# Kernel optimization log

Hardware: AMD Instinct MI355X
Metric: run time of the kernel (lower is better)

## Reference

```python
import jax, jax.numpy as jnp
import numpy as np

EPS = 1e-12  # torch F.normalize eps
K = 32       # num_clusters (hardcoded in module)

def l2norm(v, axis):
    n = jnp.sqrt(jnp.sum(v * v, axis=axis, keepdims=True))
    return v / jnp.maximum(n, EPS)

def setup_inputs() -> dict:
    key = jax.random.key(0)
    k1, k2, k3, k4 = jax.random.split(key, 4)
    B, M, D = 64, 128, 2048
    x = jax.random.normal(k1, (B, M, D), dtype=jnp.float32)
    # ragged lengths in [1, M]
    lengths = jax.random.randint(k2, (B,), 0, M, dtype=jnp.int32) + 1
    init_sc = 1.0 / np.sqrt(D)
    W = init_sc * jax.random.normal(k3, (K, D), dtype=jnp.float32)  # fc1.weight
    C = init_sc * jax.random.normal(k4, (K, D), dtype=jnp.float32)  # centroids
    return {"x": x, "lengths": lengths, "W": W, "C": C}

def reference(x, lengths, W, C):
    # x: [B,M,D] padded frames, lengths: [B] valid frame counts
    B, M, D = x.shape
    mask = (jnp.arange(M)[None, :] < lengths[:, None]).astype(x.dtype)  # [B,M]
    cnt = lengths.astype(x.dtype)[:, None]                              # [B,1]
    # avg pooling over valid (raw, un-normalized) frames
    avgpool = jnp.sum(x * mask[:, :, None], axis=1) / cnt               # [B,D]
    # per-frame L2 normalize
    xn = l2norm(x, axis=-1)                                             # [B,M,D]
    # soft assignment: linear (no bias) + softmax over clusters
    logits = jnp.einsum('bmd,kd->bmk', xn, W)
    a = jax.nn.softmax(logits, axis=-1) * mask[:, :, None]              # [B,M,K]
    # VLAD residual aggregation, GEMM form:
    # sum_m a[b,m,k]*(xn[b,m,:] - C[k,:]) = (a^T xn) - C * sum_m a
    ax = jnp.einsum('bmk,bmd->bkd', a, xn)                              # [B,K,D]
    asum = jnp.sum(a, axis=1)                                           # [B,K]
    vlad = ax - asum[:, :, None] * C[None, :, :]                        # [B,K,D]
    # intra-normalize per cluster, flatten, global L2 normalize
    vlad = l2norm(vlad, axis=2)
    vlad = vlad.reshape(B, K * D)
    vlad = l2norm(vlad, axis=1)
    return jnp.concatenate([avgpool, vlad], axis=1)                     # [B, D + K*D]
```

## Files before the change

### kernel.cpp

```cpp
#include <hip/hip_runtime.h>
#include <math.h>

#define BB 64
#define MM 128
#define DDIM 2048
#define KK 32
#define NDC 16
#define OUTROW (DDIM + KK*DDIM)

typedef __attribute__((ext_vector_type(8))) short bf16x8;
typedef __attribute__((ext_vector_type(4))) float f32x4;

__device__ __forceinline__ short f2bf(float f) {
  unsigned u = __builtin_bit_cast(unsigned, f);
  u += 0x7fffu + ((u >> 16) & 1u);
  return (short)(u >> 16);
}
__device__ __forceinline__ unsigned pack2(float lo, float hi) {
  return (unsigned)(unsigned short)f2bf(lo) | ((unsigned)(unsigned short)f2bf(hi) << 16);
}

__global__ __launch_bounds__(256) void k_prep(const float* __restrict__ W,
                                              short* __restrict__ Wb) {
  int i = (blockIdx.x * 256 + threadIdx.x) * 8;
  float4 a = *(const float4*)(W + i);
  float4 b = *(const float4*)(W + i + 4);
  bf16x8 o = {f2bf(a.x), f2bf(a.y), f2bf(a.z), f2bf(a.w),
              f2bf(b.x), f2bf(b.y), f2bf(b.z), f2bf(b.w)};
  *(bf16x8*)(Wb + i) = o;
}

__global__ __launch_bounds__(512, 4) void k_logits(const float* __restrict__ x,
    const int* __restrict__ lengths, const short* __restrict__ Wb,
    short* __restrict__ aT, float* __restrict__ asum_p) {
  const int t = threadIdx.x, wv = t >> 6, lane = t & 63;
  const int l15 = lane & 15, quad = lane >> 4;
  const int fg = blockIdx.x;
  const int g0 = fg * 16;
  const int b  = fg >> 3;
  const int m0 = (fg & 7) * 16;
  const int len = lengths[b];

  if (m0 >= len) {
    if (t < KK) asum_p[(size_t)fg * KK + t] = 0.f;
    if (t < 256) {
      const int zk = t >> 3, zoff = (t & 7) * 2;
      *(unsigned*)(aT + (size_t)b * KK * MM + (size_t)zk * MM + m0 + zoff) = 0u;
    }
    return;
  }

  const bool av = (m0 + l15) < len;
  const float* xrow = x + (size_t)(g0 + l15) * DDIM + wv * 256 + quad * 8;
  const short* w0   = Wb + l15 * DDIM + wv * 256 + quad * 8;
  const short* w1   = w0 + 16 * DDIM;

  f32x4 c0 = {0.f, 0.f, 0.f, 0.f}, c1 = {0.f, 0.f, 0.f, 0.f};
  float ssq = 0.f;
  {
    float4 xa[8], xc[8];
    bf16x8 B0[8], B1[8];
    #pragma unroll
    for (int s = 0; s < 8; ++s) {
      if (av) {
        xa[s] = *(const float4*)(xrow + s * 32);
        xc[s] = *(const float4*)(xrow + s * 32 + 4);
      } else {
        xa[s] = make_float4(0.f, 0.f, 0.f, 0.f);
        xc[s] = make_float4(0.f, 0.f, 0.f, 0.f);
      }
      B0[s] = *(const bf16x8*)(w0 + s * 32);
      B1[s] = *(const bf16x8*)(w1 + s * 32);
    }
    #pragma unroll
    for (int s = 0; s < 8; ++s) {
      ssq = fmaf(xa[s].x, xa[s].x, ssq); ssq = fmaf(xa[s].y, xa[s].y, ssq);
      ssq = fmaf(xa[s].z, xa[s].z, ssq); ssq = fmaf(xa[s].w, xa[s].w, ssq);
      ssq = fmaf(xc[s].x, xc[s].x, ssq); ssq = fmaf(xc[s].y, xc[s].y, ssq);
      ssq = fmaf(xc[s].z, xc[s].z, ssq); ssq = fmaf(xc[s].w, xc[s].w, ssq);
      bf16x8 A = {f2bf(xa[s].x), f2bf(xa[s].y), f2bf(xa[s].z), f2bf(xa[s].w),
                  f2bf(xc[s].x), f2bf(xc[s].y), f2bf(xc[s].z), f2bf(xc[s].w)};
      c0 = __builtin_amdgcn_mfma_f32_16x16x32_bf16(A, B0[s], c0, 0, 0, 0);
      c1 = __builtin_amdgcn_mfma_f32_16x16x32_bf16(A, B1[s], c1, 0, 0, 0);
    }
  }

  ssq += __shfl_xor(ssq, 16, 64);
  ssq += __shfl_xor(ssq, 32, 64);
  __shared__ float sq[8][16];
  __shared__ float lg[8][16][33];
  if (quad == 0) sq[wv][l15] = ssq;
  #pragma unroll
  for (int r = 0; r < 4; ++r) {
    lg[wv][quad * 4 + r][l15]      = c0[r];
    lg[wv][quad * 4 + r][16 + l15] = c1[r];
  }
  __syncthreads();

  const int fr = t >> 5, kk = t & 31;
  float s0 = 0.f;
  #pragma unroll
  for (int w = 0; w < 8; ++w) s0 += lg[w][fr][kk];
  float ss = 0.f;
  #pragma unroll
  for (int w = 0; w < 8; ++w) ss += sq[w][fr];
  float inv = 1.f / fmaxf(sqrtf(ss), 1e-12f);
  s0 *= inv;
  float mx = s0;
  mx = fmaxf(mx, __shfl_xor(mx, 1, 32));
  mx = fmaxf(mx, __shfl_xor(mx, 2, 32));
  mx = fmaxf(mx, __shfl_xor(mx, 4, 32));
  mx = fmaxf(mx, __shfl_xor(mx, 8, 32));
  mx = fmaxf(mx, __shfl_xor(mx, 16, 32));
  float e0 = __expf(s0 - mx);
  float se = e0;
  se += __shfl_xor(se, 1, 32);
  se += __shfl_xor(se, 2, 32);
  se += __shfl_xor(se, 4, 32);
  se += __shfl_xor(se, 8, 32);
  se += __shfl_xor(se, 16, 32);
  const bool valid = (m0 + fr) < len;
  float rr = valid ? (1.f / se) : 0.f;
  float a0 = e0 * rr;

  __syncthreads();
  lg[0][fr][kk] = a0;
  __syncthreads();
  if (t < KK) {
    float s = 0.f;
    #pragma unroll
    for (int f = 0; f < 16; ++f) s += lg[0][f][t];
    asum_p[(size_t)fg * KK + t] = s;
  }
  short* ap = aT + (size_t)b * KK * MM + m0 + fr;
  ap[(size_t)kk * MM] = f2bf(a0 * inv);
}

__global__ __launch_bounds__(256, 4) void k_vlad(const float* __restrict__ x,
    const int* __restrict__ lengths, const float* __restrict__ Cc,
    const short* __restrict__ aT, const float* __restrict__ asum_p,
    float* __restrict__ out, float* __restrict__ ssq_part) {
  const int t = threadIdx.x, wv = t >> 6, lane = t & 63;
  const int l15 = lane & 15, quad = lane >> 4;
  const int dc = blockIdx.x, b = blockIdx.y;
  const int dh = wv & 1, mh = wv >> 1;
  const int dwb = dc * 128 + dh * 64;
  const int mb  = mh * 64;
  const int len = lengths[b];

  __shared__ __attribute__((aligned(16))) char ubuf[20480];
  short (*xbt)[64][40]     = (short(*)[64][40])ubuf;
  float (*exch)[2][64][20] = (float(*)[2][64][20])ubuf;
  __shared__ float  asl[KK];
  __shared__ float4 avp[2][16];
  __shared__ float  ssw[4][17];

  if (t < KK) {
    float s = 0.f;
    #pragma unroll
    for (int p = 0; p < 8; ++p) s += asum_p[(size_t)(b * 8 + p) * KK + t];
    asl[t] = s;
  }

  const float* xb  = x  + (size_t)b * MM * DDIM;
  const short* at0 = aT + (size_t)b * KK * MM + l15 * MM + mb + quad * 8;

  const int q4   = l15 * 4;
  const int mrow = quad * 2;
  const int keyw = l15 & 3;
  const int keyr = (l15 >> 2) & 3;

  bf16x8 A0[2], A1[2];
  #pragma unroll
  for (int ms = 0; ms < 2; ++ms) {
    A0[ms] = *(const bf16x8*)(at0 + ms * 32);
    A1[ms] = *(const bf16x8*)(at0 + 16 * MM + ms * 32);
  }

  float4 v0[8], v1[8];
  #pragma unroll
  for (int ms = 0; ms < 2; ++ms) {
    #pragma unroll
    for (int p = 0; p < 4; ++p) {
      const int m = mb + ms * 32 + p * 8 + mrow;
      const float* xr = xb + (size_t)m * DDIM + dwb + q4;
      v0[ms * 4 + p] = (m < len) ? *(const float4*)xr
                                 : make_float4(0.f, 0.f, 0.f, 0.f);
      v1[ms * 4 + p] = (m + 1 < len) ? *(const float4*)(xr + DDIM)
                                     : make_float4(0.f, 0.f, 0.f, 0.f);
    }
  }

  float avg[4] = {0.f, 0.f, 0.f, 0.f};
  #pragma unroll
  for (int i = 0; i < 8; ++i) {
    avg[0] += v0[i].x + v1[i].x;
    avg[1] += v0[i].y + v1[i].y;
    avg[2] += v0[i].z + v1[i].z;
    avg[3] += v0[i].w + v1[i].w;
  }
  #pragma unroll
  for (int c = 0; c < 4; ++c) {
    avg[c] += __shfl_xor(avg[c], 16, 64);
    avg[c] += __shfl_xor(avg[c], 32, 64);
  }
  if (mh == 1 && quad == 0)
    avp[dh][l15] = make_float4(avg[0], avg[1], avg[2], avg[3]);

  f32x4 acc0[4], acc1[4];
  #pragma unroll
  for (int nt = 0; nt < 4; ++nt) {
    acc0[nt] = (f32x4){0.f, 0.f, 0.f, 0.f};
    acc1[nt] = (f32x4){0.f, 0.f, 0.f, 0.f};
  }

  #pragma unroll
  for (int ms = 0; ms < 2; ++ms) {
    #pragma unroll
    for (int p = 0; p < 4; ++p) {
      const int i = ms * 4 + p;
      const int mls = (p ^ keyw) * 8 + mrow;
      *(unsigned*)&xbt[wv][q4 + 0][mls] = pack2(v0[i].x, v1[i].x);
      *(unsigned*)&xbt[wv][q4 + 1][mls] = pack2(v0[i].y, v1[i].y);
      *(unsigned*)&xbt[wv][q4 + 2][mls] = pack2(v0[i].z, v1[i].z);
      *(unsigned*)&xbt[wv][q4 + 3][mls] = pack2(v0[i].w, v1[i].w);
    }
    #pragma unroll
    for (int nt = 0; nt < 4; ++nt) {
      bf16x8 B = *(const bf16x8*)&xbt[wv][nt * 16 + l15][(quad ^ keyr) * 8];
      acc0[nt] = __builtin_amdgcn_mfma_f32_16x16x32_bf16(A0[ms], B, acc0[nt], 0, 0, 0);
      acc1[nt] = __builtin_amdgcn_mfma_f32_16x16x32_bf16(A1[ms], B, acc1[nt], 0, 0, 0);
    }
  }

  f32x4 keep[4], give[4];
  if (mh == 0) {
    #pragma unroll
    for (int nt = 0; nt < 4; ++nt) { keep[nt] = acc0[nt]; give[nt] = acc1[nt]; }
  } else {
    #pragma unroll
    for (int nt = 0; nt < 4; ++nt) { keep[nt] = acc1[nt]; give[nt] = acc0[nt]; }
  }

  __syncthreads();
  #pragma unroll
  for (int nt = 0; nt < 4; ++nt)
    *(f32x4*)&exch[dh][mh][lane][nt * 4] = give[nt];

  if (mh == 0 && quad == 0) {
    float4 pa = avp[dh][l15];
    float rl = 1.f / (float)len;
    *(float4*)(out + (size_t)b * OUTROW + dwb + q4) =
        make_float4((avg[0] + pa.x) * rl, (avg[1] + pa.y) * rl,
                    (avg[2] + pa.z) * rl, (avg[3] + pa.w) * rl);
  }

  __syncthreads();
  #pragma unroll
  for (int nt = 0; nt < 4; ++nt)
    keep[nt] += *(const f32x4*)&exch[dh][1 - mh][lane][nt * 4];

  float* orow = out + (size_t)b * OUTROW + DDIM;
  #pragma unroll
  for (int r = 0; r < 4; ++r) {
    const int k = mh * 16 + quad * 4 + r;
    const float as = asl[k];
    float sqv = 0.f;
    #pragma unroll
    for (int nt = 0; nt < 4; ++nt) {
      const int d = dwb + nt * 16 + l15;
      float v = keep[nt][r] - as * Cc[(size_t)k * DDIM + d];
      orow[(size_t)k * DDIM + d] = v;
      sqv = fmaf(v, v, sqv);
    }
    sqv += __shfl_xor(sqv, 1, 64);
    sqv += __shfl_xor(sqv, 2, 64);
    sqv += __shfl_xor(sqv, 4, 64);
    sqv += __shfl_xor(sqv, 8, 64);
    if (l15 == 0) ssw[wv][quad * 4 + r] = sqv;
  }
  __syncthreads();
  if (t < KK) {
    const int mt = t >> 4, kl = t & 15;
    ssq_part[((size_t)dc * BB + b) * KK + t] = ssw[mt * 2][kl] + ssw[mt * 2 + 1][kl];
  }
}

__global__ __launch_bounds__(256) void k_norm(const float* __restrict__ ssq_part,
    float* __restrict__ out) {
  const int t = threadIdx.x;
  const int k = blockIdx.x;
  const int b = blockIdx.y;
  __shared__ float ssk[32];
  if (t < 32) {
    float sk = 0.f;
    #pragma unroll
    for (int dc = 0; dc < NDC; ++dc)
      sk += ssq_part[((size_t)dc * BB + b) * KK + t];
    ssk[t] = sk;
  }
  __syncthreads();
  float gss = 0.f, iv_own = 0.f;
  #pragma unroll
  for (int kk = 0; kk < 32; ++kk) {
    float nk = sqrtf(ssk[kk]);
    float iv = 1.f / fmaxf(nk, 1e-12f);
    float nn = nk * iv;
    gss += nn * nn;
    if (kk == k) iv_own = iv;
  }
  float sc = iv_own / fmaxf(sqrtf(gss), 1e-12f);
  float* row = out + (size_t)b * OUTROW + DDIM + (size_t)k * DDIM;
  #pragma unroll
  for (int h = 0; h < 2; ++h) {
    float4* p = (float4*)(row + h * 1024 + t * 4);
    float4 v = *p;
    v.x *= sc; v.y *= sc; v.z *= sc; v.w *= sc;
    *p = v;
  }
}

extern "C" void kernel_launch(void* const* d_in, const int* in_sizes, int n_in,
                              void* d_out, int out_size, void* d_ws, size_t ws_size,
                              hipStream_t stream) {
  const float* x       = (const float*)d_in[0];
  const int*   lengths = (const int*)d_in[1];
  const float* W       = (const float*)d_in[2];
  const float* C       = (const float*)d_in[3];
  float* out = (float*)d_out;

  short* Wb     = (short*)d_ws;
  short* aT     = Wb + (size_t)KK * DDIM;
  float* asum_p = (float*)(aT + (size_t)BB * KK * MM);
  float* ssqp   = asum_p + (size_t)512 * KK;

  k_prep  <<<dim3(32),      256, 0, stream>>>(W, Wb);
  k_logits<<<dim3(512),     512, 0, stream>>>(x, lengths, Wb, aT, asum_p);
  k_vlad  <<<dim3(NDC, BB), 256, 0, stream>>>(x, lengths, C, aT, asum_p, out, ssqp);
  k_norm  <<<dim3(KK, BB),  256, 0, stream>>>(ssqp, out);
}
```

Before: 143.1 us.

## Fuse all four kernels into one per-batch kernel

Replaces the prep, logits, vlad and norm kernels with one kernel that runs a single 512-thread block per batch. The block computes the soft assignments into LDS, does the VLAD GEMM with its own assignments, and applies the intra and global normalization in place. This removes three launches and the workspace round trips for the assignments, partial sums and sums of squares. In exchange the grid shrinks to only 64 blocks on a GPU with many more CUs, so each block walks all of D serially and parallelism drops sharply.

```diff
diff --git a/kernel.cpp b/kernel.cpp
--- a/kernel.cpp
+++ b/kernel.cpp
@@ -5,7 +5,6 @@
 #define MM 128
 #define DDIM 2048
 #define KK 32
-#define NDC 16
 #define OUTROW (DDIM + KK*DDIM)
 
 typedef __attribute__((ext_vector_type(8))) short bf16x8;
@@ -20,58 +19,63 @@
   return (unsigned)(unsigned short)f2bf(lo) | ((unsigned)(unsigned short)f2bf(hi) << 16);
 }
 
-__global__ __launch_bounds__(256) void k_prep(const float* __restrict__ W,
-                                              short* __restrict__ Wb) {
-  int i = (blockIdx.x * 256 + threadIdx.x) * 8;
-  float4 a = *(const float4*)(W + i);
-  float4 b = *(const float4*)(W + i + 4);
-  bf16x8 o = {f2bf(a.x), f2bf(a.y), f2bf(a.z), f2bf(a.w),
-              f2bf(b.x), f2bf(b.y), f2bf(b.z), f2bf(b.w)};
-  *(bf16x8*)(Wb + i) = o;
-}
-
-__global__ __launch_bounds__(512, 4) void k_logits(const float* __restrict__ x,
-    const int* __restrict__ lengths, const short* __restrict__ Wb,
-    short* __restrict__ aT, float* __restrict__ asum_p) {
+__global__ __launch_bounds__(512, 2) void k_all(
+    const float* __restrict__ x, const int* __restrict__ lengths,
+    const float* __restrict__ W, const float* __restrict__ Cc,
+    float* __restrict__ out) {
   const int t = threadIdx.x, wv = t >> 6, lane = t & 63;
   const int l15 = lane & 15, quad = lane >> 4;
-  const int fg = blockIdx.x;
-  const int g0 = fg * 16;
-  const int b  = fg >> 3;
-  const int m0 = (fg & 7) * 16;
+  const int b = blockIdx.x;
   const int len = lengths[b];
 
-  if (m0 >= len) {
-    if (t < KK) asum_p[(size_t)fg * KK + t] = 0.f;
-    if (t < 256) {
-      const int zk = t >> 3, zoff = (t & 7) * 2;
-      *(unsigned*)(aT + (size_t)b * KK * MM + (size_t)zk * MM + m0 + zoff) = 0u;
-    }
-    return;
-  }
-
-  const bool av = (m0 + l15) < len;
-  const float* xrow = x + (size_t)(g0 + l15) * DDIM + wv * 256 + quad * 8;
-  const short* w0   = Wb + l15 * DDIM + wv * 256 + quad * 8;
-  const short* w1   = w0 + 16 * DDIM;
-
-  f32x4 c0 = {0.f, 0.f, 0.f, 0.f}, c1 = {0.f, 0.f, 0.f, 0.f};
-  float ssq = 0.f;
+  __shared__ __attribute__((aligned(16))) char ubuf[40960];
+  float (*lg)[16][33] = (float(*)[16][33])ubuf;
+  short (*xbt)[64][40] = (short(*)[64][40])ubuf;
+  __shared__ short a_lds[KK][136];
+  __shared__ float sq[8][16];
+  __shared__ float asum_lds[KK];
+  __shared__ float ssw[8][33];
+  __shared__ float ssk[KK], scl[KK];
+
+  const float* xb = x + (size_t)b * MM * DDIM;
+  const int dwb = wv * 256;
+
+  bf16x8 WB0[8], WB1[8];
   {
-    float4 xa[8], xc[8];
-    bf16x8 B0[8], B1[8];
+    const float* w0 = W + (size_t)l15 * DDIM + dwb + quad * 8;
+    const float* w1 = w0 + (size_t)16 * DDIM;
     #pragma unroll
     for (int s = 0; s < 8; ++s) {
-      if (av) {
-        xa[s] = *(const float4*)(xrow + s * 32);
-        xc[s] = *(const float4*)(xrow + s * 32 + 4);
-      } else {
-        xa[s] = make_float4(0.f, 0.f, 0.f, 0.f);
-        xc[s] = make_float4(0.f, 0.f, 0.f, 0.f);
-      }
-      B0[s] = *(const bf16x8*)(w0 + s * 32);
-      B1[s] = *(const bf16x8*)(w1 + s * 32);
-    }
+      float4 p0 = *(const float4*)(w0 + s * 32);
+      float4 p1 = *(const float4*)(w0 + s * 32 + 4);
+      float4 q0 = *(const float4*)(w1 + s * 32);
+      float4 q1 = *(const float4*)(w1 + s * 32 + 4);
+      WB0[s] = (bf16x8){f2bf(p0.x), f2bf(p0.y), f2bf(p0.z), f2bf(p0.w),
+                        f2bf(p1.x), f2bf(p1.y), f2bf(p1.z), f2bf(p1.w)};
+      WB1[s] = (bf16x8){f2bf(q0.x), f2bf(q0.y), f2bf(q0.z), f2bf(q0.w),
+                        f2bf(q1.x), f2bf(q1.y), f2bf(q1.z), f2bf(q1.w)};
+    }
+  }
+  if (t < KK) asum_lds[t] = 0.f;
+  if (lane < 32) ssw[wv][lane] = 0.f;
+  __syncthreads();
+
+  float4 xa[8], xc[8];
+  {
+    const bool av = l15 < len;
+    const float* xr = xb + (size_t)l15 * DDIM + dwb + quad * 8;
+    #pragma unroll
+    for (int s = 0; s < 8; ++s) {
+      if (av) { xa[s] = *(const float4*)(xr + s * 32);
+                xc[s] = *(const float4*)(xr + s * 32 + 4); }
+      else    { xa[s] = make_float4(0.f, 0.f, 0.f, 0.f);
+                xc[s] = make_float4(0.f, 0.f, 0.f, 0.f); }
+    }
+  }
+  #pragma unroll
+  for (int it = 0; it < 8; ++it) {
+    f32x4 c0 = {0.f, 0.f, 0.f, 0.f}, c1 = {0.f, 0.f, 0.f, 0.f};
+    float ssq = 0.f;
     #pragma unroll
     for (int s = 0; s < 8; ++s) {
       ssq = fmaf(xa[s].x, xa[s].x, ssq); ssq = fmaf(xa[s].y, xa[s].y, ssq);
@@ -80,240 +84,184 @@
       ssq = fmaf(xc[s].z, xc[s].z, ssq); ssq = fmaf(xc[s].w, xc[s].w, ssq);
       bf16x8 A = {f2bf(xa[s].x), f2bf(xa[s].y), f2bf(xa[s].z), f2bf(xa[s].w),
                   f2bf(xc[s].x), f2bf(xc[s].y), f2bf(xc[s].z), f2bf(xc[s].w)};
-      c0 = __builtin_amdgcn_mfma_f32_16x16x32_bf16(A, B0[s], c0, 0, 0, 0);
-      c1 = __builtin_amdgcn_mfma_f32_16x16x32_bf16(A, B1[s], c1, 0, 0, 0);
-    }
-  }
-
-  ssq += __shfl_xor(ssq, 16, 64);
-  ssq += __shfl_xor(ssq, 32, 64);
-  __shared__ float sq[8][16];
-  __shared__ float lg[8][16][33];
-  if (quad == 0) sq[wv][l15] = ssq;
-  #pragma unroll
-  for (int r = 0; r < 4; ++r) {
-    lg[wv][quad * 4 + r][l15]      = c0[r];
-    lg[wv][quad * 4 + r][16 + l15] = c1[r];
-  }
-  __syncthreads();
-
-  const int fr = t >> 5, kk = t & 31;
-  float s0 = 0.f;
-  #pragma unroll
-  for (int w = 0; w < 8; ++w) s0 += lg[w][fr][kk];
-  float ss = 0.f;
-  #pragma unroll
-  for (int w = 0; w < 8; ++w) ss += sq[w][fr];
-  float inv = 1.f / fmaxf(sqrtf(ss), 1e-12f);
-  s0 *= inv;
-  float mx = s0;
-  mx = fmaxf(mx, __shfl_xor(mx, 1, 32));
-  mx = fmaxf(mx, __shfl_xor(mx, 2, 32));
-  mx = fmaxf(mx, __shfl_xor(mx, 4, 32));
-  mx = fmaxf(mx, __shfl_xor(mx, 8, 32));
-  mx = fmaxf(mx, __shfl_xor(mx, 16, 32));
-  float e0 = __expf(s0 - mx);
-  float se = e0;
-  se += __shfl_xor(se, 1, 32);
-  se += __shfl_xor(se, 2, 32);
-  se += __shfl_xor(se, 4, 32);
-  se += __shfl_xor(se, 8, 32);
-  se += __shfl_xor(se, 16, 32);
-  const bool valid = (m0 + fr) < len;
-  float rr = valid ? (1.f / se) : 0.f;
-  float a0 = e0 * rr;
-
-  __syncthreads();
-  lg[0][fr][kk] = a0;
-  __syncthreads();
-  if (t < KK) {
-    float s = 0.f;
-    #pragma unroll
-    for (int f = 0; f < 16; ++f) s += lg[0][f][t];
-    asum_p[(size_t)fg * KK + t] = s;
-  }
-  short* ap = aT + (size_t)b * KK * MM + m0 + fr;
-  ap[(size_t)kk * MM] = f2bf(a0 * inv);
-}
-
-__global__ __launch_bounds__(256, 4) void k_vlad(const float* __restrict__ x,
-    const int* __restrict__ lengths, const float* __restrict__ Cc,
-    const short* __restrict__ aT, const float* __restrict__ asum_p,
-    float* __restrict__ out, float* __restrict__ ssq_part) {
-  const int t = threadIdx.x, wv = t >> 6, lane = t & 63;
-  const int l15 = lane & 15, quad = lane >> 4;
-  const int dc = blockIdx.x, b = blockIdx.y;
-  const int dh = wv & 1, mh = wv >> 1;
-  const int dwb = dc * 128 + dh * 64;
-  const int mb  = mh * 64;
-  const int len = lengths[b];
-
-  __shared__ __attribute__((aligned(16))) char ubuf[20480];
-  short (*xbt)[64][40]     = (short(*)[64][40])ubuf;
-  float (*exch)[2][64][20] = (float(*)[2][64][20])ubuf;
-  __shared__ float  asl[KK];
-  __shared__ float4 avp[2][16];
-  __shared__ float  ssw[4][17];
-
-  if (t < KK) {
-    float s = 0.f;
-    #pragma unroll
-    for (int p = 0; p < 8; ++p) s += asum_p[(size_t)(b * 8 + p) * KK + t];
-    asl[t] = s;
-  }
-
-  const float* xb  = x  + (size_t)b * MM * DDIM;
-  const short* at0 = aT + (size_t)b * KK * MM + l15 * MM + mb + quad * 8;
+      c0 = __builtin_amdgcn_mfma_f32_16x16x32_bf16(A, WB0[s], c0, 0, 0, 0);
+      c1 = __builtin_amdgcn_mfma_f32_16x16x32_bf16(A, WB1[s], c1, 0, 0, 0);
+    }
+    float4 ya[8], yc[8];
+    if (it < 7) {
+      const int mr = (it + 1) * 16 + l15;
+      const bool av = mr < len;
+      const float* xr = xb + (size_t)mr * DDIM + dwb + quad * 8;
+      #pragma unroll
+      for (int s = 0; s < 8; ++s) {
+        if (av) { ya[s] = *(const float4*)(xr + s * 32);
+                  yc[s] = *(const float4*)(xr + s * 32 + 4); }
+        else    { ya[s] = make_float4(0.f, 0.f, 0.f, 0.f);
+                  yc[s] = make_float4(0.f, 0.f, 0.f, 0.f); }
+      }
+    }
+    ssq += __shfl_xor(ssq, 16, 64);
+    ssq += __shfl_xor(ssq, 32, 64);
+    if (quad == 0) sq[wv][l15] = ssq;
+    #pragma unroll
+    for (int r = 0; r < 4; ++r) {
+      lg[wv][quad * 4 + r][l15]      = c0[r];
+      lg[wv][quad * 4 + r][16 + l15] = c1[r];
+    }
+    __syncthreads();
+    {
+      const int fr = t >> 5, kk = t & 31;
+      float s0 = 0.f, ss = 0.f;
+      #pragma unroll
+      for (int w = 0; w < 8; ++w) { s0 += lg[w][fr][kk]; ss += sq[w][fr]; }
+      float inv = 1.f / fmaxf(sqrtf(ss), 1e-12f);
+      s0 *= inv;
+      float mx = s0;
+      mx = fmaxf(mx, __shfl_xor(mx, 1, 32));
+      mx = fmaxf(mx, __shfl_xor(mx, 2, 32));
+      mx = fmaxf(mx, __shfl_xor(mx, 4, 32));
+      mx = fmaxf(mx, __shfl_xor(mx, 8, 32));
+      mx = fmaxf(mx, __shfl_xor(mx, 16, 32));
+      float e0 = __expf(s0 - mx);
+      float se = e0;
+      se += __shfl_xor(se, 1, 32);
+      se += __shfl_xor(se, 2, 32);
+      se += __shfl_xor(se, 4, 32);
+      se += __shfl_xor(se, 8, 32);
+      se += __shfl_xor(se, 16, 32);
+      const bool valid = (it * 16 + fr) < len;
+      float rr = valid ? (1.f / se) : 0.f;
+      float a0 = e0 * rr;
+      atomicAdd(&asum_lds[kk], a0);
+      a_lds[kk][it * 16 + fr] = f2bf(a0 * inv);
+    }
+    __syncthreads();
+    #pragma unroll
+    for (int s = 0; s < 8; ++s) { xa[s] = ya[s]; xc[s] = yc[s]; }
+  }
 
   const int q4   = l15 * 4;
   const int mrow = quad * 2;
   const int keyw = l15 & 3;
   const int keyr = (l15 >> 2) & 3;
-
-  bf16x8 A0[2], A1[2];
+  const float rlen = 1.f / (float)len;
+  float* orow = out + (size_t)b * OUTROW + DDIM;
+
   #pragma unroll
-  for (int ms = 0; ms < 2; ++ms) {
-    A0[ms] = *(const bf16x8*)(at0 + ms * 32);
-    A1[ms] = *(const bf16x8*)(at0 + 16 * MM + ms * 32);
-  }
-
-  float4 v0[8], v1[8];
+  for (int dt = 0; dt < 4; ++dt) {
+    const int dbase = dwb + dt * 64;
+    f32x4 acc[2][4];
+    #pragma unroll
+    for (int kt = 0; kt < 2; ++kt)
+      #pragma unroll
+      for (int nt = 0; nt < 4; ++nt) acc[kt][nt] = (f32x4){0.f, 0.f, 0.f, 0.f};
+    float avg[4] = {0.f, 0.f, 0.f, 0.f};
+
+    #pragma unroll
+    for (int mc = 0; mc < 2; ++mc) {
+      const int mb = mc * 64;
+      float4 v0[8], v1[8];
+      #pragma unroll
+      for (int ms = 0; ms < 2; ++ms) {
+        #pragma unroll
+        for (int p = 0; p < 4; ++p) {
+          const int m = mb + ms * 32 + p * 8 + mrow;
+          const float* xr = xb + (size_t)m * DDIM + dbase + q4;
+          v0[ms * 4 + p] = (m < len) ? *(const float4*)xr
+                                     : make_float4(0.f, 0.f, 0.f, 0.f);
+          v1[ms * 4 + p] = (m + 1 < len) ? *(const float4*)(xr + DDIM)
+                                         : make_float4(0.f, 0.f, 0.f, 0.f);
+        }
+      }
+      #pragma unroll
+      for (int i = 0; i < 8; ++i) {
+        avg[0] += v0[i].x + v1[i].x;
+        avg[1] += v0[i].y + v1[i].y;
+        avg[2] += v0[i].z + v1[i].z;
+        avg[3] += v0[i].w + v1[i].w;
+      }
+      bf16x8 A0[2], A1[2];
+      #pragma unroll
+      for (int ms = 0; ms < 2; ++ms) {
+        A0[ms] = *(const bf16x8*)&a_lds[l15][mb + ms * 32 + quad * 8];
+        A1[ms] = *(const bf16x8*)&a_lds[16 + l15][mb + ms * 32 + quad * 8];
+      }
+      #pragma unroll
+      for (int ms = 0; ms < 2; ++ms) {
+        #pragma unroll
+        for (int p = 0; p < 4; ++p) {
+          const int i = ms * 4 + p;
+          const int mls = (p ^ keyw) * 8 + mrow;
+          *(unsigned*)&xbt[wv][q4 + 0][mls] = pack2(v0[i].x, v1[i].x);
+          *(unsigned*)&xbt[wv][q4 + 1][mls] = pack2(v0[i].y, v1[i].y);
+          *(unsigned*)&xbt[wv][q4 + 2][mls] = pack2(v0[i].z, v1[i].z);
+          *(unsigned*)&xbt[wv][q4 + 3][mls] = pack2(v0[i].w, v1[i].w);
+        }
+        #pragma unroll
+        for (int nt = 0; nt < 4; ++nt) {
+          bf16x8 B = *(const bf16x8*)&xbt[wv][nt * 16 + l15][(quad ^ keyr) * 8];
+          acc[0][nt] = __builtin_amdgcn_mfma_f32_16x16x32_bf16(A0[ms], B, acc[0][nt], 0, 0, 0);
+          acc[1][nt] = __builtin_amdgcn_mfma_f32_16x16x32_bf16(A1[ms], B, acc[1][nt], 0, 0, 0);
+        }
+      }
+    }
+
+    #pragma unroll
+    for (int kt = 0; kt < 2; ++kt) {
+      #pragma unroll
+      for (int r = 0; r < 4; ++r) {
+        const int k = kt * 16 + quad * 4 + r;
+        const float as = asum_lds[k];
+        float sqv = 0.f;
+        #pragma unroll
+        for (int nt = 0; nt < 4; ++nt) {
+          const int d = dbase + nt * 16 + l15;
+          float v = acc[kt][nt][r] - as * Cc[(size_t)k * DDIM + d];
+          orow[(size_t)k * DDIM + d] = v;
+          sqv = fmaf(v, v, sqv);
+        }
+        sqv += __shfl_xor(sqv, 1, 64);
+        sqv += __shfl_xor(sqv, 2, 64);
+        sqv += __shfl_xor(sqv, 4, 64);
+        sqv += __shfl_xor(sqv, 8, 64);
+        if (l15 == 0) ssw[wv][k] += sqv;
+      }
+    }
+    #pragma unroll
+    for (int c = 0; c < 4; ++c) {
+      avg[c] += __shfl_xor(avg[c], 16, 64);
+      avg[c] += __shfl_xor(avg[c], 32, 64);
+    }
+    if (quad == 0)
+      *(float4*)(out + (size_t)b * OUTROW + dbase + q4) =
+          make_float4(avg[0] * rlen, avg[1] * rlen, avg[2] * rlen, avg[3] * rlen);
+  }
+
+  __syncthreads();
+  if (t < KK) {
+    float s = 0.f;
+    #pragma unroll
+    for (int w = 0; w < 8; ++w) s += ssw[w][t];
+    ssk[t] = s;
+  }
+  __syncthreads();
+  if (t < KK) {
+    float gss = 0.f;
+    #pragma unroll
+    for (int kk = 0; kk < KK; ++kk) {
+      float nk = sqrtf(ssk[kk]);
+      float iv = 1.f / fmaxf(nk, 1e-12f);
+      float nn = nk * iv;
+      gss += nn * nn;
+    }
+    scl[t] = (1.f / fmaxf(sqrtf(gss), 1e-12f)) /
+             fmaxf(sqrtf(ssk[t]), 1e-12f);
+  }
+  __syncthreads();
   #pragma unroll
-  for (int ms = 0; ms < 2; ++ms) {
-    #pragma unroll
-    for (int p = 0; p < 4; ++p) {
-      const int m = mb + ms * 32 + p * 8 + mrow;
-      const float* xr = xb + (size_t)m * DDIM + dwb + q4;
-      v0[ms * 4 + p] = (m < len) ? *(const float4*)xr
-                                 : make_float4(0.f, 0.f, 0.f, 0.f);
-      v1[ms * 4 + p] = (m + 1 < len) ? *(const float4*)(xr + DDIM)
-                                     : make_float4(0.f, 0.f, 0.f, 0.f);
-    }
-  }
-
-  float avg[4] = {0.f, 0.f, 0.f, 0.f};
-  #pragma unroll
-  for (int i = 0; i < 8; ++i) {
-    avg[0] += v0[i].x + v1[i].x;
-    avg[1] += v0[i].y + v1[i].y;
-    avg[2] += v0[i].z + v1[i].z;
-    avg[3] += v0[i].w + v1[i].w;
-  }
-  #pragma unroll
-  for (int c = 0; c < 4; ++c) {
-    avg[c] += __shfl_xor(avg[c], 16, 64);
-    avg[c] += __shfl_xor(avg[c], 32, 64);
-  }
-  if (mh == 1 && quad == 0)
-    avp[dh][l15] = make_float4(avg[0], avg[1], avg[2], avg[3]);
-
-  f32x4 acc0[4], acc1[4];
-  #pragma unroll
-  for (int nt = 0; nt < 4; ++nt) {
-    acc0[nt] = (f32x4){0.f, 0.f, 0.f, 0.f};
-    acc1[nt] = (f32x4){0.f, 0.f, 0.f, 0.f};
-  }
-
-  #pragma unroll
-  for (int ms = 0; ms < 2; ++ms) {
-    #pragma unroll
-    for (int p = 0; p < 4; ++p) {
-      const int i = ms * 4 + p;
-      const int mls = (p ^ keyw) * 8 + mrow;
-      *(unsigned*)&xbt[wv][q4 + 0][mls] = pack2(v0[i].x, v1[i].x);
-      *(unsigned*)&xbt[wv][q4 + 1][mls] = pack2(v0[i].y, v1[i].y);
-      *(unsigned*)&xbt[wv][q4 + 2][mls] = pack2(v0[i].z, v1[i].z);
-      *(unsigned*)&xbt[wv][q4 + 3][mls] = pack2(v0[i].w, v1[i].w);
-    }
-    #pragma unroll
-    for (int nt = 0; nt < 4; ++nt) {
-      bf16x8 B = *(const bf16x8*)&xbt[wv][nt * 16 + l15][(quad ^ keyr) * 8];
-      acc0[nt] = __builtin_amdgcn_mfma_f32_16x16x32_bf16(A0[ms], B, acc0[nt], 0, 0, 0);
-      acc1[nt] = __builtin_amdgcn_mfma_f32_16x16x32_bf16(A1[ms], B, acc1[nt], 0, 0, 0);
-    }
-  }
-
-  f32x4 keep[4], give[4];
-  if (mh == 0) {
-    #pragma unroll
-    for (int nt = 0; nt < 4; ++nt) { keep[nt] = acc0[nt]; give[nt] = acc1[nt]; }
-  } else {
-    #pragma unroll
-    for (int nt = 0; nt < 4; ++nt) { keep[nt] = acc1[nt]; give[nt] = acc0[nt]; }
-  }
-
-  __syncthreads();
-  #pragma unroll
-  for (int nt = 0; nt < 4; ++nt)
-    *(f32x4*)&exch[dh][mh][lane][nt * 4] = give[nt];
-
-  if (mh == 0 && quad == 0) {
-    float4 pa = avp[dh][l15];
-    float rl = 1.f / (float)len;
-    *(float4*)(out + (size_t)b * OUTROW + dwb + q4) =
-        make_float4((avg[0] + pa.x) * rl, (avg[1] + pa.y) * rl,
-                    (avg[2] + pa.z) * rl, (avg[3] + pa.w) * rl);
-  }
-
-  __syncthreads();
-  #pragma unroll
-  for (int nt = 0; nt < 4; ++nt)
-    keep[nt] += *(const f32x4*)&exch[dh][1 - mh][lane][nt * 4];
-
-  float* orow = out + (size_t)b * OUTROW + DDIM;
-  #pragma unroll
-  for (int r = 0; r < 4; ++r) {
-    const int k = mh * 16 + quad * 4 + r;
-    const float as = asl[k];
-    float sqv = 0.f;
-    #pragma unroll
-    for (int nt = 0; nt < 4; ++nt) {
-      const int d = dwb + nt * 16 + l15;
-      float v = keep[nt][r] - as * Cc[(size_t)k * DDIM + d];
-      orow[(size_t)k * DDIM + d] = v;
-      sqv = fmaf(v, v, sqv);
-    }
-    sqv += __shfl_xor(sqv, 1, 64);
-    sqv += __shfl_xor(sqv, 2, 64);
-    sqv += __shfl_xor(sqv, 4, 64);
-    sqv += __shfl_xor(sqv, 8, 64);
-    if (l15 == 0) ssw[wv][quad * 4 + r] = sqv;
-  }
-  __syncthreads();
-  if (t < KK) {
-    const int mt = t >> 4, kl = t & 15;
-    ssq_part[((size_t)dc * BB + b) * KK + t] = ssw[mt * 2][kl] + ssw[mt * 2 + 1][kl];
-  }
-}
-
-__global__ __launch_bounds__(256) void k_norm(const float* __restrict__ ssq_part,
-    float* __restrict__ out) {
-  const int t = threadIdx.x;
-  const int k = blockIdx.x;
-  const int b = blockIdx.y;
-  __shared__ float ssk[32];
-  if (t < 32) {
-    float sk = 0.f;
-    #pragma unroll
-    for (int dc = 0; dc < NDC; ++dc)
-      sk += ssq_part[((size_t)dc * BB + b) * KK + t];
-    ssk[t] = sk;
-  }
-  __syncthreads();
-  float gss = 0.f, iv_own = 0.f;
-  #pragma unroll
-  for (int kk = 0; kk < 32; ++kk) {
-    float nk = sqrtf(ssk[kk]);
-    float iv = 1.f / fmaxf(nk, 1e-12f);
-    float nn = nk * iv;
-    gss += nn * nn;
-    if (kk == k) iv_own = iv;
-  }
-  float sc = iv_own / fmaxf(sqrtf(gss), 1e-12f);
-  float* row = out + (size_t)b * OUTROW + DDIM + (size_t)k * DDIM;
-  #pragma unroll
-  for (int h = 0; h < 2; ++h) {
-    float4* p = (float4*)(row + h * 1024 + t * 4);
+  for (int k = 0; k < KK; ++k) {
+    const float sc = scl[k];
+    float4* p = (float4*)(orow + (size_t)k * DDIM + dwb + lane * 4);
     float4 v = *p;
     v.x *= sc; v.y *= sc; v.z *= sc; v.w *= sc;
     *p = v;
@@ -329,13 +277,5 @@
   const float* C       = (const float*)d_in[3];
   float* out = (float*)d_out;
 
-  short* Wb     = (short*)d_ws;
-  short* aT     = Wb + (size_t)KK * DDIM;
-  float* asum_p = (float*)(aT + (size_t)BB * KK * MM);
-  float* ssqp   = asum_p + (size_t)512 * KK;
-
-  k_prep  <<<dim3(32),      256, 0, stream>>>(W, Wb);
-  k_logits<<<dim3(512),     512, 0, stream>>>(x, lengths, Wb, aT, asum_p);
-  k_vlad  <<<dim3(NDC, BB), 256, 0, stream>>>(x, lengths, C, aT, asum_p, out, ssqp);
-  k_norm  <<<dim3(KK, BB),  256, 0, stream>>>(ssqp, out);
-}
+  k_all<<<dim3(BB), 512, 0, stream>>>(x, lengths, W, C, out);
+}
```

Result: slower. 169.7 us (+18.6%).
